# Performance work log

Hardware: AMD Instinct MI355X
Metric: run time of the kernel (lower is better)

The kernel has to match this reference:

```python
import jax, jax.numpy as jnp
import numpy as np

B = 4096
N_DENSE = 13
N_SPARSE = 26
VOCAB = 100000
EMB = 8
CIN_SIZE = [26, 128, 128]


def setup_inputs() -> dict:
    key = jax.random.key(0)
    ks = jax.random.split(key, 24)
    s = 0.05
    dense = jax.random.normal(ks[0], (B, N_DENSE), dtype=jnp.float32)
    sparse = jax.random.randint(ks[1], (B, N_SPARSE), 0, VOCAB).astype(jnp.float32)
    inputs = jnp.concatenate([dense, sparse], axis=1)  # [B, 39]
    emb_tables = jax.random.normal(ks[2], (N_SPARSE, VOCAB, EMB), dtype=jnp.float32) * s
    linear_W = jax.random.normal(ks[3], (39, 1), dtype=jnp.float32) * s
    linear_b = jnp.zeros((1,), dtype=jnp.float32)
    # CIN Conv3d weights: kernel (H_prev, H0, 1) with out_channels H_next -> [H_next, H_prev, H0]
    W_cin0 = jax.random.normal(ks[4], (CIN_SIZE[1], CIN_SIZE[0], CIN_SIZE[0]), dtype=jnp.float32) * s
    b_cin0 = jnp.zeros((CIN_SIZE[1],), dtype=jnp.float32)
    W_cin1 = jax.random.normal(ks[5], (CIN_SIZE[2], CIN_SIZE[1], CIN_SIZE[0]), dtype=jnp.float32) * s
    b_cin1 = jnp.zeros((CIN_SIZE[2],), dtype=jnp.float32)
    cin_lin_W = jax.random.normal(ks[6], (256, 1), dtype=jnp.float32) * s
    cin_lin_b = jnp.zeros((1,), dtype=jnp.float32)
    d_W1 = jax.random.normal(ks[7], (221, 256), dtype=jnp.float32) * s
    d_b1 = jnp.zeros((256,), dtype=jnp.float32)
    d_W2 = jax.random.normal(ks[8], (256, 128), dtype=jnp.float32) * s
    d_b2 = jnp.zeros((128,), dtype=jnp.float32)
    d_W3 = jax.random.normal(ks[9], (128, 64), dtype=jnp.float32) * s
    d_b3 = jnp.zeros((64,), dtype=jnp.float32)
    d_W4 = jax.random.normal(ks[10], (64, 1), dtype=jnp.float32) * s
    d_b4 = jnp.zeros((1,), dtype=jnp.float32)
    return dict(inputs=inputs, emb_tables=emb_tables, linear_W=linear_W, linear_b=linear_b,
                W_cin0=W_cin0, b_cin0=b_cin0, W_cin1=W_cin1, b_cin1=b_cin1,
                cin_lin_W=cin_lin_W, cin_lin_b=cin_lin_b,
                d_W1=d_W1, d_b1=d_b1, d_W2=d_W2, d_b2=d_b2,
                d_W3=d_W3, d_b3=d_b3, d_W4=d_W4, d_b4=d_b4)


def reference(inputs, emb_tables, linear_W, linear_b,
              W_cin0, b_cin0, W_cin1, b_cin1, cin_lin_W, cin_lin_b,
              d_W1, d_b1, d_W2, d_b2, d_W3, d_b3, d_W4, d_b4):
    dense_in = inputs[:, :N_DENSE]                       # [B, 13]
    sparse_idx = inputs[:, N_DENSE:].astype(jnp.int32)   # [B, 26]

    # linear part over the raw inputs
    linear_out = inputs @ linear_W + linear_b            # [B, 1]

    # per-field embedding lookup: tables [F, V, E], idx [B, F] -> emb [B, F, E]
    emb = jax.vmap(lambda t, i: t[i], in_axes=(0, 1), out_axes=1)(emb_tables, sparse_idx)

    # CIN: each layer is an outer product over fields followed by a full-extent
    # Conv3d, i.e. X_{l+1}[b,o,k] = sum_{i,j} X_l[b,i,k] * X_0[b,j,k] * W[o,i,j] + b[o]
    X0 = emb
    Xi = emb
    res = []
    for W, b in ((W_cin0, b_cin0), (W_cin1, b_cin1)):
        Xi = jnp.einsum('bik,bjk,oij->bok', Xi, X0, W) + b[None, :, None]
        res.append(Xi)
    cin_feat = jnp.sum(jnp.concatenate(res, axis=1), axis=-1)  # [B, 256]
    cin_out = jax.nn.relu(cin_feat @ cin_lin_W + cin_lin_b)    # [B, 1]

    # dense MLP over [dense | flattened embeddings]
    h = jnp.concatenate([dense_in, emb.reshape(emb.shape[0], -1)], axis=1)  # [B, 221]
    h = jax.nn.relu(h @ d_W1 + d_b1)
    h = jax.nn.relu(h @ d_W2 + d_b2)
    h = jax.nn.relu(h @ d_W3 + d_b3)
    dense_out = jax.nn.relu(h @ d_W4 + d_b4)                   # [B, 1]

    return jax.nn.sigmoid(linear_out + cin_out + dense_out).reshape(-1)  # [B]
```

## Files before the change

kernel.cpp:

```cpp
#include <hip/hip_runtime.h>
#include <math.h>

#define B     4096
#define ND    13
#define NS    26
#define NF    39
#define VOCAB 100000
#define NP    351
#define NPP   360
#define CHP   45
#define GSTR  28
#define RPB   8
#define TPB   512
#define XSS   212

#define OFF_GST 0
#define OFF_CST 10080
#define OFF_C2J 10088

__global__ __launch_bounds__(256) void k_pre(const float* __restrict__ W0,
                                             const float* __restrict__ W1,
                                             const float* __restrict__ b0,
                                             const float* __restrict__ b1,
                                             const float* __restrict__ clw,
                                             float* __restrict__ Gst,
                                             float* __restrict__ cst,
                                             float* __restrict__ c2j) {
    int blk = blockIdx.x, tid = threadIdx.x;
    if (blk < 26) {
        int j = blk;
        __shared__ float vh[2][128];
        __shared__ float vj[128];
        __shared__ float c2r[2];
        {
            int i = tid & 127, h = tid >> 7;
            const float* wp = W1 + (long)(h * 64) * 3328 + i * 26 + j;
            float acc = 0.f;
#pragma unroll 8
            for (int o = 0; o < 64; o++) acc += clw[128 + h * 64 + o] * wp[o * 3328];
            vh[h][i] = acc;
        }
        __syncthreads();
        if (tid < 128) {
            float vv = vh[0][tid] + vh[1][tid];
            vj[tid] = vv;
            float c = vv * b0[tid];
            for (int off = 32; off; off >>= 1) c += __shfl_down(c, off, 64);
            if ((tid & 63) == 0) c2r[tid >> 6] = c;
        }
        __syncthreads();
        if (tid == 0) c2j[j] = c2r[0] + c2r[1];
        for (int p = tid; p < NPP; p += 256) {
            float g = 0.f;
            if (p < NP) {
                int l = 0, rem = p;
                while (rem >= NS - l) { rem -= NS - l; l++; }
                int m = l + rem;
                float sym = (l != m) ? 1.f : 0.f;
                const float* wa = W0 + l * 26 + m;
                const float* wb = W0 + m * 26 + l;
#pragma unroll 8
                for (int i = 0; i < 128; i++)
                    g += vj[i] * (wa[i * 676] + sym * wb[i * 676]);
            }
            Gst[p * GSTR + j] = g;
        }
    } else if (blk == 26) {
        for (int p = tid; p < NPP; p += 256) {
            float a = 0.f; int lmbits = 0;
            if (p < NP) {
                int l = 0, rem = p;
                while (rem >= NS - l) { rem -= NS - l; l++; }
                int m = l + rem;
                float sym = (l != m) ? 1.f : 0.f;
                const float* wa = W0 + l * 26 + m;
                const float* wb = W0 + m * 26 + l;
#pragma unroll 8
                for (int o = 0; o < 128; o++)
                    a += clw[o] * (wa[o * 676] + sym * wb[o * 676]);
                lmbits = (l << 5) | m;
            }
            Gst[p * GSTR + 26] = a;
            Gst[p * GSTR + 27] = __int_as_float(lmbits);
        }
    } else {
        __shared__ float red[2];
        float c = 0.f;
        if (tid < 128) {
            c = clw[tid] * b0[tid] + clw[128 + tid] * b1[tid];
            for (int off = 32; off; off >>= 1) c += __shfl_down(c, off, 64);
            if ((tid & 63) == 0) red[tid >> 6] = c;
        }
        __syncthreads();
        if (tid == 0) cst[0] = 8.f * (red[0] + red[1]);
    }
}

__global__ __launch_bounds__(512, 4) void k_main(
    const float* __restrict__ inputs, const float* __restrict__ tables,
    const float* __restrict__ lW, const float* __restrict__ lb,
    const float* __restrict__ Gst, const float* __restrict__ c2j,
    const float* __restrict__ cst,
    const float* __restrict__ dW1, const float* __restrict__ db1,
    const float* __restrict__ dW2, const float* __restrict__ db2,
    const float* __restrict__ dW3, const float* __restrict__ db3,
    const float* __restrict__ dW4, const float* __restrict__ db4,
    const float* __restrict__ clb,
    float* __restrict__ out) {
    __shared__ float4 sGst4[NPP * 7];
    __shared__ float insf[RPB][40];
    __shared__ float xs[RPB][XSS];
    __shared__ float inT[221][RPB];
    __shared__ float lin_s[RPB], scin_s[RPB];
    __shared__ float redbuf[8][RPB];
    __shared__ float c2s[26];

    float4* pbuf4 = sGst4;
    float*  h1T   = (float*)(sGst4 + 1024);
    float*  h2T   = (float*)(sGst4 + 1536);

    int tid = threadIdx.x;
    int b0r = blockIdx.x * RPB;

    for (int i = tid; i < NPP * 7; i += TPB) sGst4[i] = ((const float4*)Gst)[i];
    if (tid < 26) c2s[tid] = c2j[tid];
    for (int e = tid; e < RPB * NF; e += TPB) {
        int r = e / NF, c = e - r * NF;
        insf[r][c] = inputs[(b0r + r) * NF + c];
    }
    __syncthreads();

    if (tid < RPB * NS) {
        int r = tid / NS, f = tid - r * NS;
        int idx = (int)insf[r][ND + f];
        const float4* src = (const float4*)(tables + ((long)f * VOCAB + idx) * 8);
        float4 a = src[0], b4 = src[1];
        float4* dst = (float4*)&xs[r][f * 8];
        dst[0] = a; dst[1] = b4;
    }
    if (tid >= 448 && tid < 448 + RPB) {
        int r = tid - 448;
        float acc = lb[0];
        for (int c = 0; c < NF; c++) acc += insf[r][c] * lW[c];
        lin_s[r] = acc;
    }
    __syncthreads();

    for (int e = tid; e < 221 * RPB; e += TPB) {
        int c = e >> 3, r = e & 7;
        inT[c][r] = (c < ND) ? insf[r][c] : xs[r][c - ND];
    }

    {
        int lane = tid & 63, w = tid >> 6;
        int row = lane >> 3, k = lane & 7;
        const float4* grow = &sGst4[w * CHP * 7];
        float csel = (w == 0) ? 1.f : 0.f;
        const float* xrow = &xs[row][0];
        float t[27];
#pragma unroll
        for (int j = 0; j < 27; j++) t[j] = 0.f;
#pragma unroll 2
        for (int pi = 0; pi < CHP; pi++) {
            float4 g6 = grow[pi * 7 + 6];
            int lm = __float_as_int(g6.w);
            float q = xrow[(lm >> 5) * 8 + k] * xrow[(lm & 31) * 8 + k];
            float4 g0 = grow[pi * 7 + 0], g1 = grow[pi * 7 + 1];
            float4 g2 = grow[pi * 7 + 2], g3 = grow[pi * 7 + 3];
            float4 g4 = grow[pi * 7 + 4], g5 = grow[pi * 7 + 5];
            t[0]  += g0.x * q; t[1]  += g0.y * q; t[2]  += g0.z * q; t[3]  += g0.w * q;
            t[4]  += g1.x * q; t[5]  += g1.y * q; t[6]  += g1.z * q; t[7]  += g1.w * q;
            t[8]  += g2.x * q; t[9]  += g2.y * q; t[10] += g2.z * q; t[11] += g2.w * q;
            t[12] += g3.x * q; t[13] += g3.y * q; t[14] += g3.z * q; t[15] += g3.w * q;
            t[16] += g4.x * q; t[17] += g4.y * q; t[18] += g4.z * q; t[19] += g4.w * q;
            t[20] += g5.x * q; t[21] += g5.y * q; t[22] += g5.z * q; t[23] += g5.w * q;
            t[24] += g6.x * q; t[25] += g6.y * q; t[26] += g6.z * q;
        }
        float part = t[26];
#pragma unroll
        for (int j = 0; j < 26; j++) {
            float xv = xrow[j * 8 + k];
            part += (t[j] + csel * c2s[j]) * xv;
        }
        part += __shfl_xor(part, 1, 64);
        part += __shfl_xor(part, 2, 64);
        part += __shfl_xor(part, 4, 64);
        if (k == 0) redbuf[w][row] = part;
    }
    __syncthreads();

    if (tid < RPB) {
        float s = cst[0];
#pragma unroll
        for (int w = 0; w < 8; w++) s += redbuf[w][tid];
        scin_s[tid] = s;
    }
    {
        int o = tid & 255, cg = tid >> 8;
        int c0 = cg ? 111 : 0;
        int c1 = cg ? 221 : 111;
        float4 A0 = make_float4(0.f, 0.f, 0.f, 0.f);
        float4 A1 = A0;
#pragma unroll 4
        for (int c = c0; c < c1; c++) {
            float wv = dW1[c * 256 + o];
            const float4* ivp = (const float4*)&inT[c][0];
            float4 i0 = ivp[0], i1 = ivp[1];
            A0.x += i0.x * wv; A0.y += i0.y * wv; A0.z += i0.z * wv; A0.w += i0.w * wv;
            A1.x += i1.x * wv; A1.y += i1.y * wv; A1.z += i1.z * wv; A1.w += i1.w * wv;
        }
        pbuf4[cg * 512 + 0 * 256 + o] = A0;
        pbuf4[cg * 512 + 1 * 256 + o] = A1;
    }
    __syncthreads();
    if (tid < 256) {
        int o = tid;
        float bb = db1[o];
        float4 p0 = pbuf4[o],       q0 = pbuf4[512 + o];
        float4 p1 = pbuf4[256 + o], q1 = pbuf4[768 + o];
        float4 S0, S1;
        S0.x = fmaxf(p0.x + q0.x + bb, 0.f); S0.y = fmaxf(p0.y + q0.y + bb, 0.f);
        S0.z = fmaxf(p0.z + q0.z + bb, 0.f); S0.w = fmaxf(p0.w + q0.w + bb, 0.f);
        S1.x = fmaxf(p1.x + q1.x + bb, 0.f); S1.y = fmaxf(p1.y + q1.y + bb, 0.f);
        S1.z = fmaxf(p1.z + q1.z + bb, 0.f); S1.w = fmaxf(p1.w + q1.w + bb, 0.f);
        *(float4*)&h1T[o * 8]     = S0;
        *(float4*)&h1T[o * 8 + 4] = S1;
    }
    __syncthreads();

    {
        int o = tid & 127, cg = tid >> 7;
        int c0 = cg << 6;
        float4 A0 = make_float4(0.f, 0.f, 0.f, 0.f);
        float4 A1 = A0;
#pragma unroll 4
        for (int cc = 0; cc < 64; cc++) {
            int c = c0 + cc;
            float wv = dW2[c * 128 + o];
            const float4* ivp = (const float4*)&h1T[c * 8];
            float4 i0 = ivp[0], i1 = ivp[1];
            A0.x += i0.x * wv; A0.y += i0.y * wv; A0.z += i0.z * wv; A0.w += i0.w * wv;
            A1.x += i1.x * wv; A1.y += i1.y * wv; A1.z += i1.z * wv; A1.w += i1.w * wv;
        }
        pbuf4[cg * 256 + 0 * 128 + o] = A0;
        pbuf4[cg * 256 + 1 * 128 + o] = A1;
    }
    __syncthreads();
    if (tid < 128) {
        int o = tid;
        float bb = db2[o];
        float sx0 = bb, sy0 = bb, sz0 = bb, sw0 = bb;
        float sx1 = bb, sy1 = bb, sz1 = bb, sw1 = bb;
#pragma unroll
        for (int cg = 0; cg < 4; cg++) {
            float4 p0 = pbuf4[cg * 256 + o];
            float4 p1 = pbuf4[cg * 256 + 128 + o];
            sx0 += p0.x; sy0 += p0.y; sz0 += p0.z; sw0 += p0.w;
            sx1 += p1.x; sy1 += p1.y; sz1 += p1.z; sw1 += p1.w;
        }
        float4 S0, S1;
        S0.x = fmaxf(sx0, 0.f); S0.y = fmaxf(sy0, 0.f);
        S0.z = fmaxf(sz0, 0.f); S0.w = fmaxf(sw0, 0.f);
        S1.x = fmaxf(sx1, 0.f); S1.y = fmaxf(sy1, 0.f);
        S1.z = fmaxf(sz1, 0.f); S1.w = fmaxf(sw1, 0.f);
        *(float4*)&h2T[o * 8]     = S0;
        *(float4*)&h2T[o * 8 + 4] = S1;
    }
    __syncthreads();

    {
        int o = tid & 63, cg = tid >> 6;
        int c0 = cg << 4;
        float4 A0 = make_float4(0.f, 0.f, 0.f, 0.f);
        float4 A1 = A0;
#pragma unroll 8
        for (int cc = 0; cc < 16; cc++) {
            int c = c0 + cc;
            float wv = dW3[c * 64 + o];
            const float4* ivp = (const float4*)&h2T[c * 8];
            float4 i0 = ivp[0], i1 = ivp[1];
            A0.x += i0.x * wv; A0.y += i0.y * wv; A0.z += i0.z * wv; A0.w += i0.w * wv;
            A1.x += i1.x * wv; A1.y += i1.y * wv; A1.z += i1.z * wv; A1.w += i1.w * wv;
        }
        pbuf4[cg * 128 + 0 * 64 + o] = A0;
        pbuf4[cg * 128 + 1 * 64 + o] = A1;
    }
    __syncthreads();

    if (tid < 64) {
        int o = tid;
        float4 S0 = make_float4(0.f, 0.f, 0.f, 0.f);
        float4 S1 = S0;
#pragma unroll
        for (int cg = 0; cg < 8; cg++) {
            float4 p0 = pbuf4[cg * 128 + o];
            float4 p1 = pbuf4[cg * 128 + 64 + o];
            S0.x += p0.x; S0.y += p0.y; S0.z += p0.z; S0.w += p0.w;
            S1.x += p1.x; S1.y += p1.y; S1.z += p1.z; S1.w += p1.w;
        }
        float b3 = db3[o], w4 = dW4[o];
        S0.x = fmaxf(S0.x + b3, 0.f) * w4; S0.y = fmaxf(S0.y + b3, 0.f) * w4;
        S0.z = fmaxf(S0.z + b3, 0.f) * w4; S0.w = fmaxf(S0.w + b3, 0.f) * w4;
        S1.x = fmaxf(S1.x + b3, 0.f) * w4; S1.y = fmaxf(S1.y + b3, 0.f) * w4;
        S1.z = fmaxf(S1.z + b3, 0.f) * w4; S1.w = fmaxf(S1.w + b3, 0.f) * w4;
#pragma unroll
        for (int off = 1; off < 64; off <<= 1) {
            S0.x += __shfl_xor(S0.x, off, 64); S0.y += __shfl_xor(S0.y, off, 64);
            S0.z += __shfl_xor(S0.z, off, 64); S0.w += __shfl_xor(S0.w, off, 64);
            S1.x += __shfl_xor(S1.x, off, 64); S1.y += __shfl_xor(S1.y, off, 64);
            S1.z += __shfl_xor(S1.z, off, 64); S1.w += __shfl_xor(S1.w, off, 64);
        }
        if (tid == 0) {
            float sv[8] = { S0.x, S0.y, S0.z, S0.w, S1.x, S1.y, S1.z, S1.w };
            float bb = db4[0], cb = clb[0];
#pragma unroll
            for (int r = 0; r < RPB; r++) {
                float dense = fmaxf(sv[r] + bb, 0.f);
                float cin = fmaxf(scin_s[r] + cb, 0.f);
                float x = lin_s[r] + cin + dense;
                out[b0r + r] = 1.f / (1.f + expf(-x));
            }
        }
    }
}

extern "C" void kernel_launch(void* const* d_in, const int* in_sizes, int n_in,
                              void* d_out, int out_size, void* d_ws, size_t ws_size,
                              hipStream_t stream) {
    const float* inputs = (const float*)d_in[0];
    const float* tables = (const float*)d_in[1];
    const float* lW     = (const float*)d_in[2];
    const float* lb     = (const float*)d_in[3];
    const float* W0     = (const float*)d_in[4];
    const float* b0     = (const float*)d_in[5];
    const float* W1c    = (const float*)d_in[6];
    const float* b1c    = (const float*)d_in[7];
    const float* clw    = (const float*)d_in[8];
    const float* clb    = (const float*)d_in[9];
    const float* dW1    = (const float*)d_in[10];
    const float* db1    = (const float*)d_in[11];
    const float* dW2    = (const float*)d_in[12];
    const float* db2    = (const float*)d_in[13];
    const float* dW3    = (const float*)d_in[14];
    const float* db3    = (const float*)d_in[15];
    const float* dW4    = (const float*)d_in[16];
    const float* db4    = (const float*)d_in[17];

    float* ws   = (float*)d_ws;
    float* Gst  = ws + OFF_GST;
    float* cst  = ws + OFF_CST;
    float* c2j  = ws + OFF_C2J;

    k_pre<<<28, 256, 0, stream>>>(W0, W1c, b0, b1c, clw, Gst, cst, c2j);
    k_main<<<B / RPB, TPB, 0, stream>>>(inputs, tables, lW, lb, Gst, c2j, cst,
                                        dW1, db1, dW2, db2, dW3, db3, dW4, db4, clb,
                                        (float*)d_out);
}
```

Baseline: 210.4 us.

## Stream CIN weights from global, overlap gather with input load, remap MLP threads

The block no longer copies the ~40 KB Gst and c2j weight tables into LDS. The CIN loop reads them straight from global memory, using a wave-uniform (readfirstlane) base so the loads can go through the scalar/constant path. The embedding gather and the linear term now read the inputs directly, which removes one block barrier before the gather. Each MLP thread now computes two adjacent outputs for four rows using float2 weight loads. The hidden activations use a padded stride of 12 to reduce LDS bank conflicts, and the scin reduction runs alongside the layer-1 epilogue. Cutting LDS use should allow more resident blocks, at the cost of repeated global/L2 reads of Gst per block.

```diff
diff --git a/kernel.cpp b/kernel.cpp
--- a/kernel.cpp
+++ b/kernel.cpp
@@ -107,72 +107,69 @@
     const float* __restrict__ dW4, const float* __restrict__ db4,
     const float* __restrict__ clb,
     float* __restrict__ out) {
-    __shared__ float4 sGst4[NPP * 7];
     __shared__ float insf[RPB][40];
     __shared__ float xs[RPB][XSS];
-    __shared__ float inT[221][RPB];
+    __shared__ float4 inT4[448];
+    __shared__ float h1Tf[256 * 12];
+    __shared__ float4 pbuf4[1024];
     __shared__ float lin_s[RPB], scin_s[RPB];
     __shared__ float redbuf[8][RPB];
-    __shared__ float c2s[26];
-
-    float4* pbuf4 = sGst4;
-    float*  h1T   = (float*)(sGst4 + 1024);
-    float*  h2T   = (float*)(sGst4 + 1536);
+
+    float* inTf = (float*)inT4;
+    float* h2Tf = (float*)inT4;
 
     int tid = threadIdx.x;
     int b0r = blockIdx.x * RPB;
 
-    for (int i = tid; i < NPP * 7; i += TPB) sGst4[i] = ((const float4*)Gst)[i];
-    if (tid < 26) c2s[tid] = c2j[tid];
+    if (tid < RPB * NS) {
+        int r = tid / NS, f = tid - r * NS;
+        float fidx = inputs[(b0r + r) * NF + ND + f];
+        int idx = (int)fidx;
+        const float4* src = (const float4*)(tables + ((long)f * VOCAB + idx) * 8);
+        float4 a = src[0], b4 = src[1];
+        *(float4*)&xs[r][f * 8] = a;
+        *(float4*)&xs[r][f * 8 + 4] = b4;
+    }
     for (int e = tid; e < RPB * NF; e += TPB) {
         int r = e / NF, c = e - r * NF;
         insf[r][c] = inputs[(b0r + r) * NF + c];
     }
-    __syncthreads();
-
-    if (tid < RPB * NS) {
-        int r = tid / NS, f = tid - r * NS;
-        int idx = (int)insf[r][ND + f];
-        const float4* src = (const float4*)(tables + ((long)f * VOCAB + idx) * 8);
-        float4 a = src[0], b4 = src[1];
-        float4* dst = (float4*)&xs[r][f * 8];
-        dst[0] = a; dst[1] = b4;
-    }
-    if (tid >= 448 && tid < 448 + RPB) {
-        int r = tid - 448;
+    if (tid >= 496 && tid < 496 + RPB) {
+        int r = tid - 496;
         float acc = lb[0];
-        for (int c = 0; c < NF; c++) acc += insf[r][c] * lW[c];
+        for (int c = 0; c < NF; c++) acc += inputs[(b0r + r) * NF + c] * lW[c];
         lin_s[r] = acc;
     }
     __syncthreads();
 
     for (int e = tid; e < 221 * RPB; e += TPB) {
         int c = e >> 3, r = e & 7;
-        inT[c][r] = (c < ND) ? insf[r][c] : xs[r][c - ND];
-    }
-
+        inTf[c * 8 + r] = (c < ND) ? insf[r][c] : xs[r][c - ND];
+    }
     {
-        int lane = tid & 63, w = tid >> 6;
+        int w = tid >> 6;
+        int wu = __builtin_amdgcn_readfirstlane(w);
+        int lane = tid & 63;
         int row = lane >> 3, k = lane & 7;
-        const float4* grow = &sGst4[w * CHP * 7];
-        float csel = (w == 0) ? 1.f : 0.f;
+        const float4* g4 = (const float4*)Gst + wu * CHP * 7;
         const float* xrow = &xs[row][0];
+        float csel = (wu == 0) ? 1.f : 0.f;
         float t[27];
 #pragma unroll
         for (int j = 0; j < 27; j++) t[j] = 0.f;
-#pragma unroll 2
+#pragma unroll 3
         for (int pi = 0; pi < CHP; pi++) {
-            float4 g6 = grow[pi * 7 + 6];
+            float4 g6 = g4[pi * 7 + 6];
             int lm = __float_as_int(g6.w);
             float q = xrow[(lm >> 5) * 8 + k] * xrow[(lm & 31) * 8 + k];
-            float4 g0 = grow[pi * 7 + 0], g1 = grow[pi * 7 + 1];
-            float4 g2 = grow[pi * 7 + 2], g3 = grow[pi * 7 + 3];
-            float4 g4 = grow[pi * 7 + 4], g5 = grow[pi * 7 + 5];
+            float4 g0 = g4[pi * 7 + 0], g1 = g4[pi * 7 + 1];
+            float4 g2 = g4[pi * 7 + 2], g3 = g4[pi * 7 + 3];
+            float4 g4v = g4[pi * 7 + 4], g5 = g4[pi * 7 + 5];
             t[0]  += g0.x * q; t[1]  += g0.y * q; t[2]  += g0.z * q; t[3]  += g0.w * q;
             t[4]  += g1.x * q; t[5]  += g1.y * q; t[6]  += g1.z * q; t[7]  += g1.w * q;
             t[8]  += g2.x * q; t[9]  += g2.y * q; t[10] += g2.z * q; t[11] += g2.w * q;
             t[12] += g3.x * q; t[13] += g3.y * q; t[14] += g3.z * q; t[15] += g3.w * q;
-            t[16] += g4.x * q; t[17] += g4.y * q; t[18] += g4.z * q; t[19] += g4.w * q;
+            t[16] += g4v.x * q; t[17] += g4v.y * q; t[18] += g4v.z * q; t[19] += g4v.w * q;
             t[20] += g5.x * q; t[21] += g5.y * q; t[22] += g5.z * q; t[23] += g5.w * q;
             t[24] += g6.x * q; t[25] += g6.y * q; t[26] += g6.z * q;
         }
@@ -180,7 +177,7 @@
 #pragma unroll
         for (int j = 0; j < 26; j++) {
             float xv = xrow[j * 8 + k];
-            part += (t[j] + csel * c2s[j]) * xv;
+            part += (t[j] + csel * c2j[j]) * xv;
         }
         part += __shfl_xor(part, 1, 64);
         part += __shfl_xor(part, 2, 64);
@@ -189,63 +186,64 @@
     }
     __syncthreads();
 
-    if (tid < RPB) {
-        float s = cst[0];
-#pragma unroll
-        for (int w = 0; w < 8; w++) s += redbuf[w][tid];
-        scin_s[tid] = s;
-    }
     {
-        int o = tid & 255, cg = tid >> 8;
+        int p = tid & 127, h = (tid >> 7) & 1, cg = tid >> 8;
         int c0 = cg ? 111 : 0;
         int c1 = cg ? 221 : 111;
         float4 A0 = make_float4(0.f, 0.f, 0.f, 0.f);
         float4 A1 = A0;
 #pragma unroll 4
         for (int c = c0; c < c1; c++) {
-            float wv = dW1[c * 256 + o];
-            const float4* ivp = (const float4*)&inT[c][0];
-            float4 i0 = ivp[0], i1 = ivp[1];
-            A0.x += i0.x * wv; A0.y += i0.y * wv; A0.z += i0.z * wv; A0.w += i0.w * wv;
-            A1.x += i1.x * wv; A1.y += i1.y * wv; A1.z += i1.z * wv; A1.w += i1.w * wv;
-        }
-        pbuf4[cg * 512 + 0 * 256 + o] = A0;
-        pbuf4[cg * 512 + 1 * 256 + o] = A1;
-    }
-    __syncthreads();
+            float2 wv = *(const float2*)&dW1[c * 256 + 2 * p];
+            float4 iv = *(const float4*)&inTf[c * 8 + 4 * h];
+            A0.x += iv.x * wv.x; A0.y += iv.y * wv.x; A0.z += iv.z * wv.x; A0.w += iv.w * wv.x;
+            A1.x += iv.x * wv.y; A1.y += iv.y * wv.y; A1.z += iv.z * wv.y; A1.w += iv.w * wv.y;
+        }
+        pbuf4[tid * 2]     = A0;
+        pbuf4[tid * 2 + 1] = A1;
+    }
+    __syncthreads();
+
     if (tid < 256) {
         int o = tid;
         float bb = db1[o];
-        float4 p0 = pbuf4[o],       q0 = pbuf4[512 + o];
-        float4 p1 = pbuf4[256 + o], q1 = pbuf4[768 + o];
+        float4 a0 = pbuf4[o],       b0v = pbuf4[512 + o];
+        float4 a1 = pbuf4[256 + o], b1v = pbuf4[768 + o];
         float4 S0, S1;
-        S0.x = fmaxf(p0.x + q0.x + bb, 0.f); S0.y = fmaxf(p0.y + q0.y + bb, 0.f);
-        S0.z = fmaxf(p0.z + q0.z + bb, 0.f); S0.w = fmaxf(p0.w + q0.w + bb, 0.f);
-        S1.x = fmaxf(p1.x + q1.x + bb, 0.f); S1.y = fmaxf(p1.y + q1.y + bb, 0.f);
-        S1.z = fmaxf(p1.z + q1.z + bb, 0.f); S1.w = fmaxf(p1.w + q1.w + bb, 0.f);
-        *(float4*)&h1T[o * 8]     = S0;
-        *(float4*)&h1T[o * 8 + 4] = S1;
+        S0.x = fmaxf(a0.x + b0v.x + bb, 0.f); S0.y = fmaxf(a0.y + b0v.y + bb, 0.f);
+        S0.z = fmaxf(a0.z + b0v.z + bb, 0.f); S0.w = fmaxf(a0.w + b0v.w + bb, 0.f);
+        S1.x = fmaxf(a1.x + b1v.x + bb, 0.f); S1.y = fmaxf(a1.y + b1v.y + bb, 0.f);
+        S1.z = fmaxf(a1.z + b1v.z + bb, 0.f); S1.w = fmaxf(a1.w + b1v.w + bb, 0.f);
+        *(float4*)&h1Tf[o * 12]     = S0;
+        *(float4*)&h1Tf[o * 12 + 4] = S1;
+    }
+    if (tid >= 256 && tid < 256 + RPB) {
+        int r = tid - 256;
+        float s = cst[0];
+#pragma unroll
+        for (int w = 0; w < 8; w++) s += redbuf[w][r];
+        scin_s[r] = s;
     }
     __syncthreads();
 
     {
-        int o = tid & 127, cg = tid >> 7;
+        int p = tid & 63, h = (tid >> 6) & 1, cg = tid >> 7;
         int c0 = cg << 6;
         float4 A0 = make_float4(0.f, 0.f, 0.f, 0.f);
         float4 A1 = A0;
 #pragma unroll 4
         for (int cc = 0; cc < 64; cc++) {
             int c = c0 + cc;
-            float wv = dW2[c * 128 + o];
-            const float4* ivp = (const float4*)&h1T[c * 8];
-            float4 i0 = ivp[0], i1 = ivp[1];
-            A0.x += i0.x * wv; A0.y += i0.y * wv; A0.z += i0.z * wv; A0.w += i0.w * wv;
-            A1.x += i1.x * wv; A1.y += i1.y * wv; A1.z += i1.z * wv; A1.w += i1.w * wv;
-        }
-        pbuf4[cg * 256 + 0 * 128 + o] = A0;
-        pbuf4[cg * 256 + 1 * 128 + o] = A1;
-    }
-    __syncthreads();
+            float2 wv = *(const float2*)&dW2[c * 128 + 2 * p];
+            float4 iv = *(const float4*)&h1Tf[c * 12 + 4 * h];
+            A0.x += iv.x * wv.x; A0.y += iv.y * wv.x; A0.z += iv.z * wv.x; A0.w += iv.w * wv.x;
+            A1.x += iv.x * wv.y; A1.y += iv.y * wv.y; A1.z += iv.z * wv.y; A1.w += iv.w * wv.y;
+        }
+        pbuf4[tid * 2]     = A0;
+        pbuf4[tid * 2 + 1] = A1;
+    }
+    __syncthreads();
+
     if (tid < 128) {
         int o = tid;
         float bb = db2[o];
@@ -263,27 +261,27 @@
         S0.z = fmaxf(sz0, 0.f); S0.w = fmaxf(sw0, 0.f);
         S1.x = fmaxf(sx1, 0.f); S1.y = fmaxf(sy1, 0.f);
         S1.z = fmaxf(sz1, 0.f); S1.w = fmaxf(sw1, 0.f);
-        *(float4*)&h2T[o * 8]     = S0;
-        *(float4*)&h2T[o * 8 + 4] = S1;
+        *(float4*)&h2Tf[o * 12]     = S0;
+        *(float4*)&h2Tf[o * 12 + 4] = S1;
     }
     __syncthreads();
 
     {
-        int o = tid & 63, cg = tid >> 6;
+        int cg = tid >> 6, lane = tid & 63;
+        int p = lane & 31, h = lane >> 5;
         int c0 = cg << 4;
         float4 A0 = make_float4(0.f, 0.f, 0.f, 0.f);
         float4 A1 = A0;
 #pragma unroll 8
         for (int cc = 0; cc < 16; cc++) {
             int c = c0 + cc;
-            float wv = dW3[c * 64 + o];
-            const float4* ivp = (const float4*)&h2T[c * 8];
-            float4 i0 = ivp[0], i1 = ivp[1];
-            A0.x += i0.x * wv; A0.y += i0.y * wv; A0.z += i0.z * wv; A0.w += i0.w * wv;
-            A1.x += i1.x * wv; A1.y += i1.y * wv; A1.z += i1.z * wv; A1.w += i1.w * wv;
-        }
-        pbuf4[cg * 128 + 0 * 64 + o] = A0;
-        pbuf4[cg * 128 + 1 * 64 + o] = A1;
+            float2 wv = *(const float2*)&dW3[c * 64 + 2 * p];
+            float4 iv = *(const float4*)&h2Tf[c * 12 + 4 * h];
+            A0.x += iv.x * wv.x; A0.y += iv.y * wv.x; A0.z += iv.z * wv.x; A0.w += iv.w * wv.x;
+            A1.x += iv.x * wv.y; A1.y += iv.y * wv.y; A1.z += iv.z * wv.y; A1.w += iv.w * wv.y;
+        }
+        pbuf4[tid * 2]     = A0;
+        pbuf4[tid * 2 + 1] = A1;
     }
     __syncthreads();
 
```

Result: no change. 208.9 us (-0.7%).
